# Kernel tuning notes

Measured on AMD Instinct MI355X. Metric: run time of the kernel, lower is better.

## Reference

```python
import jax, jax.numpy as jnp
import numpy as np
from jax import lax

B, N, D = 64, 499, 256          # batch, nodes(=seq_len), emb_size
NUM_P, NUM_Q, NUM_C = 10000, 2000, 10


def _seg_softmax(e, dst, n):
    # e: [E,H] edge scores, segment softmax over destination node
    m = jax.ops.segment_max(e, dst, num_segments=n)
    ex = jnp.exp(e - m[dst])
    s = jax.ops.segment_sum(ex, dst, num_segments=n)
    return ex / s[dst]


def gat_conv(x, src, dst, W, a_src, a_dst, b, concat):
    # x: [B,n,Fin], W: [Fin,H*Fo], a_src/a_dst: [H,Fo], b: [H*Fo] or [Fo]
    Bn, n, _ = x.shape
    H, Fo = a_src.shape
    h = (x @ W).reshape(Bn, n, H, Fo)
    es = jnp.einsum('bnhf,hf->bnh', h, a_src)
    ed = jnp.einsum('bnhf,hf->bnh', h, a_dst)
    e = jax.nn.leaky_relu(es[:, src] + ed[:, dst], 0.2)   # [B,E,H]
    alpha = jax.vmap(lambda eb: _seg_softmax(eb, dst, n))(e)
    msg = alpha[..., None] * h[:, src]                    # [B,E,H,Fo]
    out = jax.vmap(lambda mb: jax.ops.segment_sum(mb, dst, num_segments=n))(msg)
    out = out.reshape(Bn, n, H * Fo) if concat else out.mean(axis=2)
    return out + b


def lstm(xs, W_ih, W_hh, b_ih, b_hh):
    # xs: [B,S,I]; torch gate order i,f,g,o
    Bn = xs.shape[0]
    Hd = W_hh.shape[1]

    def step(carry, xt):
        h, c = carry
        g = xt @ W_ih.T + b_ih + h @ W_hh.T + b_hh
        i, f, gg, o = jnp.split(g, 4, axis=-1)
        c = jax.nn.sigmoid(f) * c + jax.nn.sigmoid(i) * jnp.tanh(gg)
        h = jax.nn.sigmoid(o) * jnp.tanh(c)
        return (h, c), h

    init = (jnp.zeros((Bn, Hd), xs.dtype), jnp.zeros((Bn, Hd), xs.dtype))
    _, hs = lax.scan(step, init, xs.transpose(1, 0, 2))
    return hs.transpose(1, 0, 2)


def _edges():
    # genr_edge_index(true_length-1=498): chain over nodes 0..497, then
    # PyG GATConv removes self-loops and adds them back for all 499 nodes.
    L = N - 1
    src, dst = [], []
    for i in range(L):
        for j in (i - 1, i + 1):
            if 0 <= j < L:
                src.append(i)
                dst.append(j)
    src += list(range(N))
    dst += list(range(N))
    return np.array(src, np.int32), np.array(dst, np.int32)


def setup_inputs() -> dict:
    key = jax.random.key(0)
    ks = jax.random.split(key, 30)
    f32 = jnp.float32

    def nrm(k, shape, s=0.05):
        return jax.random.normal(k, shape, dtype=f32) * s

    src, dst = _edges()
    inp = {
        'true_length': jnp.full((B,), N, dtype=jnp.int32),
        'p': jax.random.randint(ks[0], (B, N), 0, NUM_P + 1, dtype=jnp.int32),
        'q': jax.random.randint(ks[1], (B, N), 0, NUM_Q + 1, dtype=jnp.int32),
        'r': jax.random.randint(ks[2], (B, N), 0, 2, dtype=jnp.int32),
        'aff': jax.random.randint(ks[3], (B, N), 0, NUM_C + 1, dtype=jnp.int32),
        'q_next': jax.random.randint(ks[4], (B, N), 0, NUM_Q + 1, dtype=jnp.int32),
        'p_next': jax.random.randint(ks[5], (B, N), 0, NUM_P + 1, dtype=jnp.int32),
        'src': jnp.asarray(src),
        'dst': jnp.asarray(dst),
        'emb_p': nrm(ks[6], (NUM_P + 1, D), 1.0),
        'emb_q': nrm(ks[7], (NUM_Q + 1, D), 1.0),
        'emb_r': nrm(ks[8], (2, D), 1.0),
        'emb_aff': nrm(ks[9], (NUM_C + 1, D), 1.0),
        'W_affcat': nrm(ks[10], (2 * D, D)),
        'b_affcat': nrm(ks[11], (D,)),
        'W_g1': nrm(ks[12], (D, 8 * 128)),
        'a_src1': nrm(ks[13], (8, 128)),
        'a_dst1': nrm(ks[14], (8, 128)),
        'b_g1': nrm(ks[15], (8 * 128,)),
        'W_g2': nrm(ks[16], (8 * 128, D)),
        'a_src2': nrm(ks[17], (1, D)),
        'a_dst2': nrm(ks[18], (1, D)),
        'b_g2': nrm(ks[19], (D,)),
        'W_ih': nrm(ks[20], (4 * D, 4 * D)),
        'W_hh': nrm(ks[21], (4 * D, D)),
        'b_ih': nrm(ks[22], (4 * D,)),
        'b_hh': nrm(ks[23], (4 * D,)),
        'W_out': nrm(ks[24], (3 * D, 1)),
        'b_out': nrm(ks[25], (1,)),
    }
    return inp


def reference(true_length, p, q, r, aff, q_next, p_next, src, dst,
              emb_p, emb_q, emb_r, emb_aff, W_affcat, b_affcat,
              W_g1, a_src1, a_dst1, b_g1, W_g2, a_src2, a_dst2, b_g2,
              W_ih, W_hh, b_ih, b_hh, W_out, b_out):
    # eval mode: all dropouts are identity
    p_emb = emb_p[p]            # [B,N,D]
    q_emb = emb_q[q]
    r_emb = emb_r[r]
    qn_emb = emb_q[q_next]
    pn_emb = emb_p[p_next]
    aff_emb = emb_aff[aff]

    x = jnp.concatenate([p_emb, aff_emb], axis=-1) @ W_affcat + b_affcat
    x = jax.nn.elu(gat_conv(x, src, dst, W_g1, a_src1, a_dst1, b_g1, True))
    x = gat_conv(x, src, dst, W_g2, a_src2, a_dst2, b_g2, False)   # [B,N,D]

    seq = jnp.concatenate([p_emb, q_emb, r_emb, x], axis=-1)       # [B,N,4D]
    h = lstm(seq, W_ih, W_hh, b_ih, b_hh)                          # [B,N,D]
    y = jnp.concatenate([h, qn_emb, pn_emb], axis=-1) @ W_out + b_out
    return jax.nn.sigmoid(y)
```

## Files before the change

kernel.cpp:

```cpp
#include <hip/hip_runtime.h>
#include <hip/hip_bf16.h>

typedef unsigned int u32;
typedef unsigned short u16;

#define MTOT 31936
#define NN 499
#define BB 64

__device__ __forceinline__ float lo16(u32 u){ return __uint_as_float(u << 16); }
__device__ __forceinline__ float hi16(u32 u){ return __uint_as_float(u & 0xffff0000u); }
__device__ __forceinline__ float bf2f(u16 u){ return __uint_as_float(((u32)u) << 16); }
__device__ __forceinline__ u16 f2bf(float f){
  u32 x = __float_as_uint(f);
  u32 r = (x + 0x7fffu + ((x >> 16) & 1u)) >> 16;
  return (u16)r;
}
__device__ __forceinline__ float sigf(float x){ return 1.f / (1.f + __expf(-x)); }
__device__ __forceinline__ float tanh_(float x){ return 2.f * sigf(2.f * x) - 1.f; }
__device__ __forceinline__ float wred(float v){
  #pragma unroll
  for (int off = 32; off; off >>= 1) v += __shfl_down(v, off, 64);
  return v;
}

typedef __attribute__((ext_vector_type(2))) __bf16 bf16x2;
#if __has_builtin(__builtin_amdgcn_fdot2_f32_bf16)
__device__ __forceinline__ float dot2bf(u32 w, u32 h, float acc){
  union { u32 u; bf16x2 v; } uw, uh;
  uw.u = w; uh.u = h;
  return __builtin_amdgcn_fdot2_f32_bf16(uw.v, uh.v, acc, false);
}
#else
__device__ __forceinline__ float dot2bf(u32 w, u32 h, float acc){
  return acc + lo16(w) * lo16(h) + hi16(w) * hi16(h);
}
#endif

#if __has_builtin(__builtin_amdgcn_cvt_pk_bf16_f32)
__device__ __forceinline__ u32 pk2bf(float a, float b){
  union { bf16x2 v; u32 u; } r;
  r.v = __builtin_amdgcn_cvt_pk_bf16_f32(a, b);
  return r.u;
}
#else
__device__ __forceinline__ u32 pk2bf(float a, float b){
  return (u32)f2bf(a) | ((u32)f2bf(b) << 16);
}
#endif

typedef __attribute__((ext_vector_type(8))) short bfrag8;
typedef __attribute__((ext_vector_type(4))) float f4_t;
union FragU { uint4 u; bfrag8 s; };

__device__ __forceinline__ f4_t mfma16(FragU a, FragU b, f4_t c){
  return __builtin_amdgcn_mfma_f32_16x16x32_bf16(a.s, b.s, c, 0, 0, 0);
}

template <typename AL>
__device__ __forceinline__ void gemm_core2(int K32, const uint4* __restrict__ Bpack,
                                           f4_t (&acc)[4][2], AL aload){
  __shared__ __align__(16) uint4 As[2][256];
  const int tid = threadIdx.x;
  const int wave = tid >> 6, lane = tid & 63;
  const uint4* Bp0 = Bpack + ((size_t)(blockIdx.y * 8 + wave * 2) * K32) * 64 + lane;
  const uint4* Bp1 = Bp0 + (size_t)K32 * 64;
  int buf = 0;
  for (int kt = 0; kt < K32; kt++){
    FragU b0, b1;
    b0.u = Bp0[kt * 64];
    b1.u = Bp1[kt * 64];
    As[buf][tid] = aload(kt);
    __syncthreads();
    FragU a0, a1, a2, a3;
    a0.u = As[buf][lane];
    a1.u = As[buf][64 + lane];
    a2.u = As[buf][128 + lane];
    a3.u = As[buf][192 + lane];
    acc[0][0] = mfma16(a0, b0, acc[0][0]); acc[0][1] = mfma16(a0, b1, acc[0][1]);
    acc[1][0] = mfma16(a1, b0, acc[1][0]); acc[1][1] = mfma16(a1, b1, acc[1][1]);
    acc[2][0] = mfma16(a2, b0, acc[2][0]); acc[2][1] = mfma16(a2, b1, acc[2][1]);
    acc[3][0] = mfma16(a3, b0, acc[3][0]); acc[3][1] = mfma16(a3, b1, acc[3][1]);
    buf ^= 1;
  }
}

__global__ __launch_bounds__(256) void k_packB(const float* __restrict__ W, u16* __restrict__ out,
                                               int K, int N, int trans){
  int c = blockIdx.x * 256 + threadIdx.x;
  int K32 = K >> 5;
  int total = (N >> 4) * K32 * 64;
  if (c >= total) return;
  int l = c & 63;
  int rem = c >> 6;
  int kt = rem % K32, nt = rem / K32;
  int n = nt * 16 + (l & 15);
  int kb = kt * 32 + (l >> 4) * 8;
  u32 ov[4];
  #pragma unroll
  for (int j2 = 0; j2 < 4; j2++){
    int k = kb + j2 * 2;
    float f0 = trans ? W[(size_t)n * K + k]     : W[(size_t)k * N + n];
    float f1 = trans ? W[(size_t)n * K + k + 1] : W[(size_t)(k + 1) * N + n];
    ov[j2] = pk2bf(f0, f1);
  }
  uint4 o; o.x = ov[0]; o.y = ov[1]; o.z = ov[2]; o.w = ov[3];
  *(uint4*)(out + (size_t)c * 8) = o;
}

__global__ void k_csr(const int* __restrict__ src, const int* __restrict__ dst, int E,
                      int* __restrict__ deg, int* __restrict__ insrc){
  int tid = threadIdx.x;
  for (int i = tid; i < NN; i += 256) deg[i] = 0;
  for (int i = tid; i < NN * 4; i += 256) insrc[i] = 0;
  __syncthreads();
  for (int e = tid; e < E; e += 256){
    int d = dst[e];
    int slot = atomicAdd(&deg[d], 1);
    if (slot < 4) insrc[d * 4 + slot] = src[e];
  }
}

__global__ void k_packwhh(const float* __restrict__ Whh, uint4* __restrict__ whh4){
  int idx = blockIdx.x * 256 + threadIdx.x;
  int j = idx & 1023, kc = idx >> 10;
  const float* w = Whh + (size_t)j * 256 + kc * 8;
  float4 w0 = *(const float4*)w;
  float4 w1 = *(const float4*)(w + 4);
  uint4 o;
  o.x = pk2bf(w0.x, w0.y);
  o.y = pk2bf(w0.z, w0.w);
  o.z = pk2bf(w1.x, w1.y);
  o.w = pk2bf(w1.z, w1.w);
  whh4[kc * 1024 + j] = o;
}

__global__ __launch_bounds__(256) void k_affcat_m(
    const float* __restrict__ emb_p, const float* __restrict__ emb_aff,
    const int* __restrict__ p, const int* __restrict__ aff,
    const uint4* __restrict__ Bpack, const float* __restrict__ bias, float* __restrict__ C){
  const int tid = threadIdx.x;
  const int mBase = blockIdx.x * 64, nBase = blockIdx.y * 128;
  const int ls = tid & 63;
  const int gm = mBase + (tid >> 6) * 16 + (ls & 15);
  const int kqoff = (ls >> 4) * 8;
  const float* rp = emb_p + (size_t)p[gm] * 256 + kqoff;
  const float* ra = emb_aff + (size_t)aff[gm] * 256 + kqoff;
  f4_t acc[4][2] = {};
  gemm_core2(16, Bpack, acc, [&](int kt) -> uint4 {
    int kb = kt * 32;
    const float* s = (kb < 256) ? (rp + kb) : (ra + kb - 256);
    float4 v0 = *(const float4*)s;
    float4 v1 = *(const float4*)(s + 4);
    uint4 o; o.x = pk2bf(v0.x, v0.y); o.y = pk2bf(v0.z, v0.w);
    o.z = pk2bf(v1.x, v1.y); o.w = pk2bf(v1.z, v1.w);
    return o;
  });
  const int wave = tid >> 6, lane = tid & 63;
  const int rb = (lane >> 4) << 2;
  const int cbase = nBase + wave * 32 + (lane & 15);
  float b0 = bias[cbase], b1 = bias[cbase + 16];
  #pragma unroll
  for (int i = 0; i < 4; i++)
    #pragma unroll
    for (int r = 0; r < 4; r++){
      int row = mBase + i * 16 + rb + r;
      C[(size_t)row * 256 + cbase]      = acc[i][0][r] + b0;
      C[(size_t)row * 256 + cbase + 16] = acc[i][1][r] + b1;
    }
}

__global__ __launch_bounds__(256) void k_h1_m(const float* __restrict__ A,
                                              const uint4* __restrict__ Bpack,
                                              u16* __restrict__ Cb){
  const int tid = threadIdx.x;
  const int mBase = blockIdx.x * 64, nBase = blockIdx.y * 128;
  const int ls = tid & 63;
  const int gm = mBase + (tid >> 6) * 16 + (ls & 15);
  const float* ra = A + (size_t)gm * 256 + (ls >> 4) * 8;
  f4_t acc[4][2] = {};
  gemm_core2(8, Bpack, acc, [&](int kt) -> uint4 {
    const float* s = ra + kt * 32;
    float4 v0 = *(const float4*)s;
    float4 v1 = *(const float4*)(s + 4);
    uint4 o; o.x = pk2bf(v0.x, v0.y); o.y = pk2bf(v0.z, v0.w);
    o.z = pk2bf(v1.x, v1.y); o.w = pk2bf(v1.z, v1.w);
    return o;
  });
  const int wave = tid >> 6, lane = tid & 63;
  const int rb = (lane >> 4) << 2;
  const int cbase = nBase + wave * 32 + (lane & 15);
  #pragma unroll
  for (int i = 0; i < 4; i++)
    #pragma unroll
    for (int r = 0; r < 4; r++){
      int row = mBase + i * 16 + rb + r;
      Cb[(size_t)row * 1024 + cbase]      = f2bf(acc[i][0][r]);
      Cb[(size_t)row * 1024 + cbase + 16] = f2bf(acc[i][1][r]);
    }
}

__global__ __launch_bounds__(256) void k_h2_m(const u16* __restrict__ A,
                                              const uint4* __restrict__ Bpack,
                                              float* __restrict__ C){
  const int tid = threadIdx.x;
  const int mBase = blockIdx.x * 64, nBase = blockIdx.y * 128;
  const int ls = tid & 63;
  const int gm = mBase + (tid >> 6) * 16 + (ls & 15);
  const u16* ra = A + (size_t)gm * 1024 + (ls >> 4) * 8;
  f4_t acc[4][2] = {};
  gemm_core2(32, Bpack, acc, [&](int kt) -> uint4 {
    return *(const uint4*)(ra + kt * 32);
  });
  const int wave = tid >> 6, lane = tid & 63;
  const int rb = (lane >> 4) << 2;
  const int cbase = nBase + wave * 32 + (lane & 15);
  #pragma unroll
  for (int i = 0; i < 4; i++)
    #pragma unroll
    for (int r = 0; r < 4; r++){
      int row = mBase + i * 16 + rb + r;
      C[(size_t)row * 256 + cbase]      = acc[i][0][r];
      C[(size_t)row * 256 + cbase + 16] = acc[i][1][r];
    }
}

__global__ __launch_bounds__(256) void k_gates_m(
    const float* __restrict__ emb_p, const float* __restrict__ emb_q, const float* __restrict__ emb_r,
    const int* __restrict__ p, const int* __restrict__ q, const int* __restrict__ r,
    const float* __restrict__ x2, const uint4* __restrict__ Bpack,
    const float* __restrict__ bih, const float* __restrict__ bhh, u16* __restrict__ Cb){
  const int tid = threadIdx.x;
  const int mBase = blockIdx.x * 64, nBase = blockIdx.y * 128;
  const int ls = tid & 63;
  const int gm = mBase + (tid >> 6) * 16 + (ls & 15);
  const int kqoff = (ls >> 4) * 8;
  const float* s0 = emb_p + (size_t)p[gm] * 256 + kqoff;
  const float* s1 = emb_q + (size_t)q[gm] * 256 + kqoff;
  const float* s2 = emb_r + (size_t)r[gm] * 256 + kqoff;
  const float* s3 = x2 + (size_t)gm * 256 + kqoff;
  f4_t acc[4][2] = {};
  gemm_core2(32, Bpack, acc, [&](int kt) -> uint4 {
    int kb = kt * 32;
    int seg = kb >> 8, ko = kb & 255;
    const float* s = (seg == 0) ? s0 : ((seg == 1) ? s1 : ((seg == 2) ? s2 : s3));
    float4 v0 = *(const float4*)(s + ko);
    float4 v1 = *(const float4*)(s + ko + 4);
    uint4 o; o.x = pk2bf(v0.x, v0.y); o.y = pk2bf(v0.z, v0.w);
    o.z = pk2bf(v1.x, v1.y); o.w = pk2bf(v1.z, v1.w);
    return o;
  });
  const int wave = tid >> 6, lane = tid & 63;
  const int rb = (lane >> 4) << 2;
  const int cbase = nBase + wave * 32 + (lane & 15);
  float b0 = bih[cbase] + bhh[cbase];
  float b1 = bih[cbase + 16] + bhh[cbase + 16];
  #pragma unroll
  for (int i = 0; i < 4; i++)
    #pragma unroll
    for (int r2 = 0; r2 < 4; r2++){
      int row = mBase + i * 16 + rb + r2;
      Cb[(size_t)row * 1024 + cbase]      = f2bf(acc[i][0][r2] + b0);
      Cb[(size_t)row * 1024 + cbase + 16] = f2bf(acc[i][1][r2] + b1);
    }
}

__global__ __launch_bounds__(256) void k_esed(
    const u16* __restrict__ hb, const float* __restrict__ hf,
    const float* __restrict__ asrc, const float* __restrict__ adst,
    float* __restrict__ es, float* __restrict__ ed, int Hm1, int Fo){
  int w = blockIdx.x * 4 + (threadIdx.x >> 6);
  int lane = threadIdx.x & 63;
  int h = w & Hm1;
  size_t base = (size_t)w * Fo;
  float s = 0.f, d = 0.f;
  for (int f = lane; f < Fo; f += 64){
    float hv = hb ? bf2f(hb[base + f]) : hf[base + f];
    s += hv * asrc[h * Fo + f];
    d += hv * adst[h * Fo + f];
  }
  s = wred(s); d = wred(d);
  if (!lane){ es[w] = s; ed[w] = d; }
}

__global__ __launch_bounds__(256) void k_gatagg(
    const u16* __restrict__ hb, const float* __restrict__ hf,
    const float* __restrict__ es, const float* __restrict__ ed,
    const int* __restrict__ deg, const int* __restrict__ insrc,
    const float* __restrict__ bias, u16* __restrict__ outb, float* __restrict__ outf,
    int H, int foShift, int HFo, int do_elu){
  int m = blockIdx.x;
  int b = m / NN;
  int n = m - b * NN;
  int dg = deg[n];
  int s0 = insrc[n * 4 + 0];
  int s1 = insrc[n * 4 + 1];
  int s2 = insrc[n * 4 + 2];
  int rowBase = b * NN;
  for (int c = threadIdx.x; c < HFo; c += 256){
    int h = c >> foShift;
    float edv = ed[(size_t)m * H + h];
    float sc0 = es[(size_t)(rowBase + s0) * H + h] + edv;
    sc0 = (sc0 >= 0.f) ? sc0 : 0.2f * sc0;
    float sc1 = 0.f, sc2 = 0.f, mx = sc0;
    if (dg > 1){ sc1 = es[(size_t)(rowBase + s1) * H + h] + edv; sc1 = (sc1 >= 0.f) ? sc1 : 0.2f * sc1; mx = fmaxf(mx, sc1); }
    if (dg > 2){ sc2 = es[(size_t)(rowBase + s2) * H + h] + edv; sc2 = (sc2 >= 0.f) ? sc2 : 0.2f * sc2; mx = fmaxf(mx, sc2); }
    float e0 = __expf(sc0 - mx), e1 = 0.f, e2 = 0.f;
    if (dg > 1) e1 = __expf(sc1 - mx);
    if (dg > 2) e2 = __expf(sc2 - mx);
    float inv = 1.f / (e0 + e1 + e2);
    size_t c0 = (size_t)(rowBase + s0) * HFo + c;
    float acc = e0 * (hb ? bf2f(hb[c0]) : hf[c0]);
    if (dg > 1){ size_t c1 = (size_t)(rowBase + s1) * HFo + c; acc += e1 * (hb ? bf2f(hb[c1]) : hf[c1]); }
    if (dg > 2){ size_t c2 = (size_t)(rowBase + s2) * HFo + c; acc += e2 * (hb ? bf2f(hb[c2]) : hf[c2]); }
    acc *= inv;
    float o = acc + bias[c];
    if (do_elu) o = (o > 0.f) ? o : (__expf(o) - 1.f);
    if (outb) outb[(size_t)m * HFo + c] = f2bf(o);
    else      outf[(size_t)m * HFo + c] = o;
  }
}

#define KREG 18
#define KLDS 9
__global__ __launch_bounds__(1024)
__attribute__((amdgpu_waves_per_eu(1, 4)))
void k_lstm(const u16* __restrict__ gates,
            const uint4* __restrict__ whh4,
            float* __restrict__ h_all){
  __shared__ __align__(16) uint4 wlds[KLDS][1024];
  __shared__ __align__(16) u32 h2_lds[128];
  __shared__ float dots[1024];
  const int b = blockIdx.x, t = threadIdx.x;
  const int lane = t & 63;
  float c = 0.f;
  if (t < 128) h2_lds[t] = 0;
  uint4 wreg[KREG];
  #pragma unroll
  for (int kc = 0; kc < KREG; kc++) wreg[kc] = whh4[kc * 1024 + t];
  #pragma unroll
  for (int kc = 0; kc < KLDS; kc++) wlds[kc][t] = whh4[(KREG + kc) * 1024 + t];
  __syncthreads();
  const u16* gb = gates + (size_t)b * NN * 1024;
  const uint4* wbase = whh4 + (KREG + KLDS) * 1024 + t;
  for (int n = 0; n < NN; n++){
    uint4 hvec = *(const uint4*)&h2_lds[(lane & 31) * 4];
    float acc0 = bf2f(gb[(size_t)n * 1024 + t]);
    float acc1 = 0.f;
    #pragma unroll
    for (int i = 0; i < 32 - KREG - KLDS; i++){
      const int kc = KREG + KLDS + i;
      uint4 w = wbase[i * 1024];
      u32 hx = (u32)__builtin_amdgcn_readlane((int)hvec.x, kc);
      u32 hy = (u32)__builtin_amdgcn_readlane((int)hvec.y, kc);
      u32 hz = (u32)__builtin_amdgcn_readlane((int)hvec.z, kc);
      u32 hw = (u32)__builtin_amdgcn_readlane((int)hvec.w, kc);
      acc0 = dot2bf(w.x, hx, acc0);
      acc1 = dot2bf(w.y, hy, acc1);
      acc0 = dot2bf(w.z, hz, acc0);
      acc1 = dot2bf(w.w, hw, acc1);
    }
    #pragma unroll
    for (int i = 0; i < KLDS; i++){
      const int kc = KREG + i;
      uint4 w = wlds[i][t];
      u32 hx = (u32)__builtin_amdgcn_readlane((int)hvec.x, kc);
      u32 hy = (u32)__builtin_amdgcn_readlane((int)hvec.y, kc);
      u32 hz = (u32)__builtin_amdgcn_readlane((int)hvec.z, kc);
      u32 hw = (u32)__builtin_amdgcn_readlane((int)hvec.w, kc);
      acc0 = dot2bf(w.x, hx, acc0);
      acc1 = dot2bf(w.y, hy, acc1);
      acc0 = dot2bf(w.z, hz, acc0);
      acc1 = dot2bf(w.w, hw, acc1);
    }
    #pragma unroll
    for (int kc = 0; kc < KREG; kc++){
      uint4 w = wreg[kc];
      u32 hx = (u32)__builtin_amdgcn_readlane((int)hvec.x, kc);
      u32 hy = (u32)__builtin_amdgcn_readlane((int)hvec.y, kc);
      u32 hz = (u32)__builtin_amdgcn_readlane((int)hvec.z, kc);
      u32 hw = (u32)__builtin_amdgcn_readlane((int)hvec.w, kc);
      acc0 = dot2bf(w.x, hx, acc0);
      acc1 = dot2bf(w.y, hy, acc1);
      acc0 = dot2bf(w.z, hz, acc0);
      acc1 = dot2bf(w.w, hw, acc1);
    }
    dots[t] = acc0 + acc1;
    __syncthreads();
    if (t < 256){
      float ai = dots[t], af = dots[256 + t], ag = dots[512 + t], ao = dots[768 + t];
      c = sigf(af) * c + sigf(ai) * tanh_(ag);
      float h = sigf(ao) * tanh_(c);
      h_all[((size_t)b * NN + n) * 256 + t] = h;
      ((u16*)h2_lds)[t] = f2bf(h);
    }
    __syncthreads();
  }
}

__global__ __launch_bounds__(256) void k_out(const float* __restrict__ h_all,
    const float* __restrict__ emb_q, const float* __restrict__ emb_p,
    const int* __restrict__ qn, const int* __restrict__ pn,
    const float* __restrict__ Wo, const float* __restrict__ bo, float* __restrict__ y){
  int m = blockIdx.x * 4 + (threadIdx.x >> 6);
  int lane = threadIdx.x & 63;
  const float* hr = h_all + (size_t)m * 256;
  const float* rq = emb_q + (size_t)qn[m] * 256;
  const float* rp = emb_p + (size_t)pn[m] * 256;
  float acc = 0.f;
  #pragma unroll
  for (int f = 0; f < 256; f += 64){
    int d = f + lane;
    acc += hr[d] * Wo[d];
    acc += rq[d] * Wo[256 + d];
    acc += rp[d] * Wo[512 + d];
  }
  acc = wred(acc);
  if (!lane) y[m] = sigf(acc + bo[0]);
}

extern "C" void kernel_launch(void* const* d_in, const int* in_sizes, int n_in,
                              void* d_out, int out_size, void* d_ws, size_t ws_size,
                              hipStream_t stream){
  (void)n_in; (void)out_size; (void)ws_size;
  const int* p    = (const int*)d_in[1];
  const int* q    = (const int*)d_in[2];
  const int* r    = (const int*)d_in[3];
  const int* aff  = (const int*)d_in[4];
  const int* qn   = (const int*)d_in[5];
  const int* pn   = (const int*)d_in[6];
  const int* src  = (const int*)d_in[7];
  const int* dst  = (const int*)d_in[8];
  const float* emb_p  = (const float*)d_in[9];
  const float* emb_q  = (const float*)d_in[10];
  const float* emb_r  = (const float*)d_in[11];
  const float* emb_aff= (const float*)d_in[12];
  const float* W_aff  = (const float*)d_in[13];
  const float* b_aff  = (const float*)d_in[14];
  const float* W_g1   = (const float*)d_in[15];
  const float* a_s1   = (const float*)d_in[16];
  const float* a_d1   = (const float*)d_in[17];
  const float* b_g1   = (const float*)d_in[18];
  const float* W_g2   = (const float*)d_in[19];
  const float* a_s2   = (const float*)d_in[20];
  const float* a_d2   = (const float*)d_in[21];
  const float* b_g2   = (const float*)d_in[22];
  const float* W_ih   = (const float*)d_in[23];
  const float* W_hh   = (const float*)d_in[24];
  const float* b_ih   = (const float*)d_in[25];
  const float* b_hh   = (const float*)d_in[26];
  const float* W_out  = (const float*)d_in[27];
  const float* b_out  = (const float*)d_in[28];
  const int E = in_sizes[7];

  char* ws = (char*)d_ws;
  size_t off = 0;
  auto alloc = [&](size_t bytes){ size_t ret = off; off += (bytes + 255) & ~(size_t)255; return ret; };
  size_t o_bigA = alloc((size_t)MTOT * 1024 * 2);
  size_t o_bigB = alloc((size_t)MTOT * 1024 * 2);
  size_t o_buf3 = alloc((size_t)MTOT * 256 * 4);
  size_t o_es1 = alloc((size_t)MTOT * 8 * 4);
  size_t o_ed1 = alloc((size_t)MTOT * 8 * 4);
  size_t o_es2 = alloc((size_t)MTOT * 4);
  size_t o_ed2 = alloc((size_t)MTOT * 4);
  size_t o_whh = alloc((size_t)32 * 1024 * 16);
  size_t o_deg = alloc(512 * 4);
  size_t o_ins = alloc((size_t)NN * 4 * 4);
  size_t o_bpih  = alloc((size_t)131072 * 16);
  size_t o_bpg1  = alloc((size_t)32768 * 16);
  size_t o_bpg2  = alloc((size_t)32768 * 16);
  size_t o_bpaff = alloc((size_t)16384 * 16);

  u16*   h1    = (u16*)(ws + o_bigA);
  u16*   gates = (u16*)(ws + o_bigA);
  u16*   g1out = (u16*)(ws + o_bigB);
  float* x2    = (float*)(ws + o_bigB);
  float* x0    = (float*)(ws + o_buf3);
  float* h2    = (float*)(ws + o_buf3);
  float* h_all = (float*)(ws + o_buf3);
  float* es1   = (float*)(ws + o_es1);
  float* ed1   = (float*)(ws + o_ed1);
  float* es2   = (float*)(ws + o_es2);
  float* ed2   = (float*)(ws + o_ed2);
  uint4* whh4  = (uint4*)(ws + o_whh);
  int*   degp  = (int*)(ws + o_deg);
  int*   insp  = (int*)(ws + o_ins);
  u16*   bpih  = (u16*)(ws + o_bpih);
  u16*   bpg1  = (u16*)(ws + o_bpg1);
  u16*   bpg2  = (u16*)(ws + o_bpg2);
  u16*   bpaff = (u16*)(ws + o_bpaff);

  k_csr<<<1, 256, 0, stream>>>(src, dst, E, degp, insp);
  k_packwhh<<<128, 256, 0, stream>>>(W_hh, whh4);
  k_packB<<<512, 256, 0, stream>>>(W_ih, bpih, 1024, 1024, 1);
  k_packB<<<128, 256, 0, stream>>>(W_g1, bpg1, 256, 1024, 0);
  k_packB<<<128, 256, 0, stream>>>(W_g2, bpg2, 1024, 256, 0);
  k_packB<<<64, 256, 0, stream>>>(W_aff, bpaff, 512, 256, 0);

  k_affcat_m<<<dim3(NN, 2), 256, 0, stream>>>(emb_p, emb_aff, p, aff,
                                              (const uint4*)bpaff, b_aff, x0);
  k_h1_m<<<dim3(NN, 8), 256, 0, stream>>>(x0, (const uint4*)bpg1, h1);
  k_esed<<<(MTOT * 8) / 4, 256, 0, stream>>>(h1, nullptr, a_s1, a_d1, es1, ed1, 7, 128);
  k_gatagg<<<MTOT, 256, 0, stream>>>(h1, nullptr, es1, ed1, degp, insp, b_g1,
                                     g1out, nullptr, 8, 7, 1024, 1);
  k_h2_m<<<dim3(NN, 2), 256, 0, stream>>>(g1out, (const uint4*)bpg2, h2);
  k_esed<<<MTOT / 4, 256, 0, stream>>>(nullptr, h2, a_s2, a_d2, es2, ed2, 0, 256);
  k_gatagg<<<MTOT, 256, 0, stream>>>(nullptr, h2, es2, ed2, degp, insp, b_g2,
                                     nullptr, x2, 1, 8, 256, 0);
  k_gates_m<<<dim3(NN, 8), 256, 0, stream>>>(emb_p, emb_q, emb_r, p, q, r, x2,
                                             (const uint4*)bpih, b_ih, b_hh, gates);
  k_lstm<<<BB, 1024, 0, stream>>>(gates, whh4, h_all);
  k_out<<<MTOT / 4, 256, 0, stream>>>(h_all, emb_q, emb_p, qn, pn, W_out, b_out, (float*)d_out);
}
```

Baseline: 1.780 ms.

## Batch LSTM recurrence across 16 sequences per block using MFMA

Measured after the change: 6.259 ms. 3.52x slower.

```diff
diff --git a/kernel.cpp b/kernel.cpp
--- a/kernel.cpp
+++ b/kernel.cpp
@@ -25,17 +25,6 @@
 }
 
 typedef __attribute__((ext_vector_type(2))) __bf16 bf16x2;
-#if __has_builtin(__builtin_amdgcn_fdot2_f32_bf16)
-__device__ __forceinline__ float dot2bf(u32 w, u32 h, float acc){
-  union { u32 u; bf16x2 v; } uw, uh;
-  uw.u = w; uh.u = h;
-  return __builtin_amdgcn_fdot2_f32_bf16(uw.v, uh.v, acc, false);
-}
-#else
-__device__ __forceinline__ float dot2bf(u32 w, u32 h, float acc){
-  return acc + lo16(w) * lo16(h) + hi16(w) * hi16(h);
-}
-#endif
 
 #if __has_builtin(__builtin_amdgcn_cvt_pk_bf16_f32)
 __device__ __forceinline__ u32 pk2bf(float a, float b){
@@ -59,11 +48,11 @@
 
 template <typename AL>
 __device__ __forceinline__ void gemm_core2(int K32, const uint4* __restrict__ Bpack,
-                                           f4_t (&acc)[4][2], AL aload){
+                                           int ntBase, f4_t (&acc)[4][2], AL aload){
   __shared__ __align__(16) uint4 As[2][256];
   const int tid = threadIdx.x;
-  const int wave = tid >> 6, lane = tid & 63;
-  const uint4* Bp0 = Bpack + ((size_t)(blockIdx.y * 8 + wave * 2) * K32) * 64 + lane;
+  const int lane = tid & 63;
+  const uint4* Bp0 = Bpack + ((size_t)ntBase * K32) * 64 + lane;
   const uint4* Bp1 = Bp0 + (size_t)K32 * 64;
   int buf = 0;
   for (int kt = 0; kt < K32; kt++){
@@ -121,20 +110,6 @@
   }
 }
 
-__global__ void k_packwhh(const float* __restrict__ Whh, uint4* __restrict__ whh4){
-  int idx = blockIdx.x * 256 + threadIdx.x;
-  int j = idx & 1023, kc = idx >> 10;
-  const float* w = Whh + (size_t)j * 256 + kc * 8;
-  float4 w0 = *(const float4*)w;
-  float4 w1 = *(const float4*)(w + 4);
-  uint4 o;
-  o.x = pk2bf(w0.x, w0.y);
-  o.y = pk2bf(w0.z, w0.w);
-  o.z = pk2bf(w1.x, w1.y);
-  o.w = pk2bf(w1.z, w1.w);
-  whh4[kc * 1024 + j] = o;
-}
-
 __global__ __launch_bounds__(256) void k_affcat_m(
     const float* __restrict__ emb_p, const float* __restrict__ emb_aff,
     const int* __restrict__ p, const int* __restrict__ aff,
@@ -147,7 +122,7 @@
   const float* rp = emb_p + (size_t)p[gm] * 256 + kqoff;
   const float* ra = emb_aff + (size_t)aff[gm] * 256 + kqoff;
   f4_t acc[4][2] = {};
-  gemm_core2(16, Bpack, acc, [&](int kt) -> uint4 {
+  gemm_core2(16, Bpack, blockIdx.y * 8 + ((tid >> 6) << 1), acc, [&](int kt) -> uint4 {
     int kb = kt * 32;
     const float* s = (kb < 256) ? (rp + kb) : (ra + kb - 256);
     float4 v0 = *(const float4*)s;
@@ -179,7 +154,7 @@
   const int gm = mBase + (tid >> 6) * 16 + (ls & 15);
   const float* ra = A + (size_t)gm * 256 + (ls >> 4) * 8;
   f4_t acc[4][2] = {};
-  gemm_core2(8, Bpack, acc, [&](int kt) -> uint4 {
+  gemm_core2(8, Bpack, blockIdx.y * 8 + ((tid >> 6) << 1), acc, [&](int kt) -> uint4 {
     const float* s = ra + kt * 32;
     float4 v0 = *(const float4*)s;
     float4 v1 = *(const float4*)(s + 4);
@@ -209,7 +184,7 @@
   const int gm = mBase + (tid >> 6) * 16 + (ls & 15);
   const u16* ra = A + (size_t)gm * 1024 + (ls >> 4) * 8;
   f4_t acc[4][2] = {};
-  gemm_core2(32, Bpack, acc, [&](int kt) -> uint4 {
+  gemm_core2(32, Bpack, blockIdx.y * 8 + ((tid >> 6) << 1), acc, [&](int kt) -> uint4 {
     return *(const uint4*)(ra + kt * 32);
   });
   const int wave = tid >> 6, lane = tid & 63;
@@ -240,7 +215,7 @@
   const float* s2 = emb_r + (size_t)r[gm] * 256 + kqoff;
   const float* s3 = x2 + (size_t)gm * 256 + kqoff;
   f4_t acc[4][2] = {};
-  gemm_core2(32, Bpack, acc, [&](int kt) -> uint4 {
+  gemm_core2(32, Bpack, blockIdx.y * 8 + ((tid >> 6) << 1), acc, [&](int kt) -> uint4 {
     int kb = kt * 32;
     int seg = kb >> 8, ko = kb & 255;
     const float* s = (seg == 0) ? s0 : ((seg == 1) ? s1 : ((seg == 2) ? s2 : s3));
@@ -263,6 +238,40 @@
       Cb[(size_t)row * 1024 + cbase]      = f2bf(acc[i][0][r2] + b0);
       Cb[(size_t)row * 1024 + cbase + 16] = f2bf(acc[i][1][r2] + b1);
     }
+}
+
+__global__ __launch_bounds__(256) void k_repack(const u16* __restrict__ gates,
+                                                u16* __restrict__ G0L){
+  __shared__ __align__(16) u16 staged[64][128];
+  const int tid = threadIdx.x;
+  const int n = blockIdx.x, w = blockIdx.y;
+  #pragma unroll
+  for (int i = 0; i < 4; i++){
+    const int c = tid + i * 256;
+    const int b = c >> 4, seg = c & 15;
+    const int t = seg >> 1, cc8 = (seg & 1) * 8;
+    const int g = t & 3, ut = t >> 2;
+    const u16* srcp = gates + (size_t)(b * NN + n) * 1024 + g * 256 + w * 32 + ut * 16 + cc8;
+    *(uint4*)&staged[b][seg * 8] = *(const uint4*)srcp;
+  }
+  __syncthreads();
+  const int Lt = tid >> 2, qq = tid & 3;
+  const int mhi = (Lt >> 4) << 2;
+  const int cc = Lt & 15;
+  #pragma unroll
+  for (int bg = 0; bg < 4; bg++){
+    u32 vw[4];
+    #pragma unroll
+    for (int j = 0; j < 4; j++){
+      const int t = 2 * qq + (j >> 1);
+      const int r0 = (2 * j) & 3;
+      const u16 lo = staged[bg * 16 + mhi + r0][t * 16 + cc];
+      const u16 hi = staged[bg * 16 + mhi + r0 + 1][t * 16 + cc];
+      vw[j] = (u32)lo | ((u32)hi << 16);
+    }
+    uint4 o; o.x = vw[0]; o.y = vw[1]; o.z = vw[2]; o.w = vw[3];
+    *(uint4*)(G0L + ((((size_t)(bg * NN + n) * 8 + w) * 64 + Lt) * 32 + qq * 8)) = o;
+  }
 }
 
 __global__ __launch_bounds__(256) void k_esed(
@@ -321,80 +330,91 @@
   }
 }
 
-#define KREG 18
-#define KLDS 9
-__global__ __launch_bounds__(1024)
-__attribute__((amdgpu_waves_per_eu(1, 4)))
-void k_lstm(const u16* __restrict__ gates,
-            const uint4* __restrict__ whh4,
+__global__ __launch_bounds__(512)
+void k_lstm(const u16* __restrict__ g0l,
+            const uint4* __restrict__ bph,
             float* __restrict__ h_all){
-  __shared__ __align__(16) uint4 wlds[KLDS][1024];
-  __shared__ __align__(16) u32 h2_lds[128];
-  __shared__ float dots[1024];
-  const int b = blockIdx.x, t = threadIdx.x;
-  const int lane = t & 63;
-  float c = 0.f;
-  if (t < 128) h2_lds[t] = 0;
-  uint4 wreg[KREG];
-  #pragma unroll
-  for (int kc = 0; kc < KREG; kc++) wreg[kc] = whh4[kc * 1024 + t];
-  #pragma unroll
-  for (int kc = 0; kc < KLDS; kc++) wlds[kc][t] = whh4[(KREG + kc) * 1024 + t];
+  __shared__ __align__(16) u16 hsh[2][4096];
+  const int bg = blockIdx.x, tid = threadIdx.x;
+  const int w = tid >> 6, lane = tid & 63;
+  const int am = lane & 15, oct = lane >> 4;
+  const int hm = oct << 2, uc = am;
+  const u32 abNos = (u32)(am * 512 + oct * 16);
+  const u32 sw = (u32)((am & 7) << 4);
+  ((uint4*)hsh[1])[tid] = make_uint4(0u, 0u, 0u, 0u);
+
+  const uint4* wp[8];
+  #pragma unroll
+  for (int t = 0; t < 8; t++){
+    const int nt = (t & 3) * 16 + w * 2 + (t >> 2);
+    wp[t] = bph + (size_t)(nt * 8) * 64 + lane;
+  }
+  uint4 wbuf[3][8];
+  #pragma unroll
+  for (int s = 0; s < 3; s++)
+    #pragma unroll
+    for (int t = 0; t < 8; t++) wbuf[s][t] = wp[t][s * 64];
+
+  const uint4* g0p = (const uint4*)g0l + ((size_t)((size_t)bg * NN * 8 + w) * 64 + lane) * 4;
+  uint4 G0q[4];
+  G0q[0] = g0p[0]; G0q[1] = g0p[1]; G0q[2] = g0p[2]; G0q[3] = g0p[3];
+  g0p += 2048;
+
+  const size_t hofs0 = ((size_t)(bg * 16 + hm) * NN) * 256 + (size_t)w * 32 + uc;
+  float cst[8] = {0.f, 0.f, 0.f, 0.f, 0.f, 0.f, 0.f, 0.f};
   __syncthreads();
-  const u16* gb = gates + (size_t)b * NN * 1024;
-  const uint4* wbase = whh4 + (KREG + KLDS) * 1024 + t;
+
+  #pragma unroll 1
   for (int n = 0; n < NN; n++){
-    uint4 hvec = *(const uint4*)&h2_lds[(lane & 31) * 4];
-    float acc0 = bf2f(gb[(size_t)n * 1024 + t]);
-    float acc1 = 0.f;
-    #pragma unroll
-    for (int i = 0; i < 32 - KREG - KLDS; i++){
-      const int kc = KREG + KLDS + i;
-      uint4 w = wbase[i * 1024];
-      u32 hx = (u32)__builtin_amdgcn_readlane((int)hvec.x, kc);
-      u32 hy = (u32)__builtin_amdgcn_readlane((int)hvec.y, kc);
-      u32 hz = (u32)__builtin_amdgcn_readlane((int)hvec.z, kc);
-      u32 hw = (u32)__builtin_amdgcn_readlane((int)hvec.w, kc);
-      acc0 = dot2bf(w.x, hx, acc0);
-      acc1 = dot2bf(w.y, hy, acc1);
-      acc0 = dot2bf(w.z, hz, acc0);
-      acc1 = dot2bf(w.w, hw, acc1);
-    }
-    #pragma unroll
-    for (int i = 0; i < KLDS; i++){
-      const int kc = KREG + i;
-      uint4 w = wlds[i][t];
-      u32 hx = (u32)__builtin_amdgcn_readlane((int)hvec.x, kc);
-      u32 hy = (u32)__builtin_amdgcn_readlane((int)hvec.y, kc);
-      u32 hz = (u32)__builtin_amdgcn_readlane((int)hvec.z, kc);
-      u32 hw = (u32)__builtin_amdgcn_readlane((int)hvec.w, kc);
-      acc0 = dot2bf(w.x, hx, acc0);
-      acc1 = dot2bf(w.y, hy, acc1);
-      acc0 = dot2bf(w.z, hz, acc0);
-      acc1 = dot2bf(w.w, hw, acc1);
-    }
-    #pragma unroll
-    for (int kc = 0; kc < KREG; kc++){
-      uint4 w = wreg[kc];
-      u32 hx = (u32)__builtin_amdgcn_readlane((int)hvec.x, kc);
-      u32 hy = (u32)__builtin_amdgcn_readlane((int)hvec.y, kc);
-      u32 hz = (u32)__builtin_amdgcn_readlane((int)hvec.z, kc);
-      u32 hw = (u32)__builtin_amdgcn_readlane((int)hvec.w, kc);
-      acc0 = dot2bf(w.x, hx, acc0);
-      acc1 = dot2bf(w.y, hy, acc1);
-      acc0 = dot2bf(w.z, hz, acc0);
-      acc1 = dot2bf(w.w, hw, acc1);
-    }
-    dots[t] = acc0 + acc1;
-    __syncthreads();
-    if (t < 256){
-      float ai = dots[t], af = dots[256 + t], ag = dots[512 + t], ao = dots[768 + t];
-      c = sigf(af) * c + sigf(ai) * tanh_(ag);
-      float h = sigf(ao) * tanh_(c);
-      h_all[((size_t)b * NN + n) * 256 + t] = h;
-      ((u16*)h2_lds)[t] = f2bf(h);
-    }
-    __syncthreads();
+    const char* hrd = (const char*)hsh[(n + 1) & 1];
+    char* hwr = (char*)hsh[n & 1];
+    FragU a[8];
+    #pragma unroll
+    for (int kc = 0; kc < 8; kc++)
+      a[kc].u = *(const uint4*)(hrd + ((abNos + (u32)(kc * 64)) ^ sw));
+    f4_t acc[8] = {};
+    #pragma unroll
+    for (int pp = 0; pp < 8; pp++){
+      const int slot = pp % 3;
+      const int gnext = (pp + 3 < 8) ? (pp + 3) : slot;
+      #pragma unroll
+      for (int t = 0; t < 8; t++){
+        FragU b; b.u = wbuf[slot][t];
+        acc[t] = mfma16(a[pp], b, acc[t]);
+      }
+      #pragma unroll
+      for (int t = 0; t < 8; t++) wbuf[slot][t] = wp[t][gnext * 64];
+    }
+    #pragma unroll
+    for (int ut = 0; ut < 2; ut++){
+      #pragma unroll
+      for (int rr = 0; rr < 4; rr++){
+        float gv[4];
+        #pragma unroll
+        for (int g = 0; g < 4; g++){
+          const int t = ut * 4 + g;
+          const uint4 qv = G0q[t >> 1];
+          const int wi = ((t & 1) << 1) + (rr >> 1);
+          const u32 uw = (wi == 0) ? qv.x : (wi == 1) ? qv.y : (wi == 2) ? qv.z : qv.w;
+          gv[g] = acc[t][rr] + ((rr & 1) ? hi16(uw) : lo16(uw));
+        }
+        const int ci = ut * 4 + rr;
+        const float cv = sigf(gv[1]) * cst[ci] + sigf(gv[0]) * tanh_(gv[2]);
+        cst[ci] = cv;
+        const float hv = sigf(gv[3]) * tanh_(cv);
+        const int mm = hm + rr;
+        const u32 wb = ((u32)(mm * 512 + (w * 32 + ut * 16 + uc) * 2)) ^ ((u32)(mm & 7) << 4);
+        *(u16*)(hwr + wb) = f2bf(hv);
+        h_all[hofs0 + (size_t)rr * (NN * 256) + (size_t)n * 256 + ut * 16] = hv;
+      }
+    }
+    if (n + 1 < NN){
+      G0q[0] = g0p[0]; G0q[1] = g0p[1]; G0q[2] = g0p[2]; G0q[3] = g0p[3];
+      g0p += 2048;
+    }
+    asm volatile("s_waitcnt lgkmcnt(0)" ::: "memory");
+    __builtin_amdgcn_s_barrier();
+    __builtin_amdgcn_sched_barrier(0);
   }
 }
 
@@ -463,7 +483,7 @@
   size_t o_ed1 = alloc((size_t)MTOT * 8 * 4);
   size_t o_es2 = alloc((size_t)MTOT * 4);
   size_t o_ed2 = alloc((size_t)MTOT * 4);
-  size_t o_whh = alloc((size_t)32 * 1024 * 16);
+  size_t o_whh = alloc((size_t)32768 * 16);
   size_t o_deg = alloc(512 * 4);
   size_t o_ins = alloc((size_t)NN * 4 * 4);
   size_t o_bpih  = alloc((size_t)131072 * 16);
@@ -475,6 +495,7 @@
   u16*   gates = (u16*)(ws + o_bigA);
   u16*   g1out = (u16*)(ws + o_bigB);
   float* x2    = (float*)(ws + o_bigB);
+  u16*   G0L   = (u16*)(ws + o_bigB);
   float* x0    = (float*)(ws + o_buf3);
   float* h2    = (float*)(ws + o_buf3);
   float* h_all = (float*)(ws + o_buf3);
@@ -482,7 +503,7 @@
   float* ed1   = (float*)(ws + o_ed1);
   float* es2   = (float*)(ws + o_es2);
   float* ed2   = (float*)(ws + o_ed2);
-  uint4* whh4  = (uint4*)(ws + o_whh);
+  u16*   bphh  = (u16*)(ws + o_whh);
   int*   degp  = (int*)(ws + o_deg);
   int*   insp  = (int*)(ws + o_ins);
   u16*   bpih  = (u16*)(ws + o_bpih);
@@ -491,7 +512,7 @@
   u16*   bpaff = (u16*)(ws + o_bpaff);
 
   k_csr<<<1, 256, 0, stream>>>(src, dst, E, degp, insp);
-  k_packwhh<<<128, 256, 0, stream>>>(W_hh, whh4);
+  k_packB<<<128, 256, 0, stream>>>(W_hh, bphh, 256, 1024, 1);
   k_packB<<<512, 256, 0, stream>>>(W_ih, bpih, 1024, 1024, 1);
   k_packB<<<128, 256, 0, stream>>>(W_g1, bpg1, 256, 1024, 0);
   k_packB<<<128, 256, 0, stream>>>(W_g2, bpg2, 1024, 256, 0);
@@ -509,6 +530,7 @@
                                      nullptr, x2, 1, 8, 256, 0);
   k_gates_m<<<dim3(NN, 8), 256, 0, stream>>>(emb_p, emb_q, emb_r, p, q, r, x2,
                                              (const uint4*)bpih, b_ih, b_hh, gates);
-  k_lstm<<<BB, 1024, 0, stream>>>(gates, whh4, h_all);
+  k_repack<<<dim3(NN, 8), 256, 0, stream>>>(gates, G0L);
+  k_lstm<<<4, 512, 0, stream>>>(G0L, (const uint4*)bphh, h_all);
   k_out<<<MTOT / 4, 256, 0, stream>>>(h_all, emb_q, emb_p, qn, pn, W_out, b_out, (float*)d_out);
 }
```
